# Kernel optimization log

Hardware: AMD Instinct MI355X
Metric: run time of the kernel (lower is better)

Reference implementation:

```python
import jax, jax.numpy as jnp
from jax import lax
import numpy as np

BS, HID, INP, NSPAN, NOUT, NUM_DAYS = 4096, 1024, 512, 8, 2, 20


def setup_inputs() -> dict:
    key = jax.random.key(0)
    ks = jax.random.split(key, 12)
    s = 1.0 / np.sqrt(HID)  # torch default uniform(-1/sqrt(hid), 1/sqrt(hid))
    u = lambda k, shape: jax.random.uniform(k, shape, jnp.float32, -s, s)
    return {
        "hx": jax.random.normal(ks[0], (BS, HID), jnp.float32),
        "cx": jax.random.normal(ks[1], (BS, HID), jnp.float32),
        "W_ih": u(ks[2], (4 * HID, INP)),
        "W_hh": u(ks[3], (4 * HID, HID)),
        "b_ih": u(ks[4], (4 * HID,)),
        "b_hh": u(ks[5], (4 * HID,)),
        "W_fcin": u(ks[6], (INP, HID)),
        "b_fcin": u(ks[7], (INP,)),
        "W_fcout": u(ks[8], (NOUT, HID)),
        "b_fcout": u(ks[9], (NOUT,)),
        "W_span": u(ks[10], (NSPAN, HID)),
        "b_span": u(ks[11], (NSPAN,)),
    }


def reference(hx, cx, W_ih, W_hh, b_ih, b_hh, W_fcin, b_fcin, W_fcout, b_fcout, W_span, b_span):
    # num-span head on the initial hidden state
    num_spans = jax.nn.softmax(hx @ W_span.T + b_span, axis=-1)  # [B, NSPAN]

    def step(carry, _):
        h, c, inp = carry
        gates = inp @ W_ih.T + b_ih + h @ W_hh.T + b_hh  # [B, 4H]
        i, f, g, o = jnp.split(gates, 4, axis=-1)  # torch LSTMCell gate order i,f,g,o
        c = jax.nn.sigmoid(f) * c + jax.nn.sigmoid(i) * jnp.tanh(g)
        h = jax.nn.sigmoid(o) * jnp.tanh(c)
        inp = jax.nn.relu(h @ W_fcin.T + b_fcin)  # next-step input
        out = jax.nn.softmax(h @ W_fcout.T + b_fcout, axis=-1)  # [B, 2]
        return (h, c, inp), out

    inp0 = jnp.zeros((hx.shape[0], W_ih.shape[1]), hx.dtype)
    _, outs = lax.scan(step, (hx, cx, inp0), None, length=NUM_DAYS)  # [T, B, 2]
    outputs = jnp.transpose(outs, (1, 0, 2))  # [B, T, 2]
    return num_spans, outputs
```

## Files before the change

kernel.cpp:

```cpp
#include <hip/hip_runtime.h>

typedef __bf16 bf16x8 __attribute__((ext_vector_type(8)));
typedef float f32x4 __attribute__((ext_vector_type(4)));
typedef unsigned short ushort_t;
typedef unsigned short u16x8 __attribute__((ext_vector_type(8)));

#define BSZ 4096
#define HID 1024
#define INPD 512
#define NSPAN 8
#define NOUT 2
#define NDAYS 20
#define XLD 1536


__device__ __forceinline__ ushort_t f2bf(float f) {
  union { float f; unsigned u; } v; v.f = f;
  unsigned r = v.u + 0x7FFFu + ((v.u >> 16) & 1u);
  return (ushort_t)(r >> 16);
}
__device__ __forceinline__ float bf2f(ushort_t b) {
  union { unsigned u; float f; } v; v.u = ((unsigned)b) << 16;
  return v.f;
}
__device__ __forceinline__ float sigf(float x) { return 1.f / (1.f + __expf(-x)); }
__device__ __forceinline__ float tanhfast(float x) { return 2.f / (1.f + __expf(-2.f * x)) - 1.f; }

__device__ __forceinline__ void gload16(const void* g, void* l) {
  __builtin_amdgcn_global_load_lds((const __attribute__((address_space(1))) void*)g,
                                   (__attribute__((address_space(3))) void*)l, 16, 0, 0);
}

__global__ void prep_gates_w(const float* __restrict__ Wih, const float* __restrict__ Whh,
                             const float* __restrict__ bih, const float* __restrict__ bhh,
                             ushort_t* __restrict__ Wgf, float* __restrict__ bg) {
  int gid = blockIdx.x * 256 + threadIdx.x;
  int rb = gid / 3072;
  int rem = gid - rb * 3072;
  int kk = rem >> 6;
  int li = rem & 63;
  int rp = rb * 16 + (li & 15);
  int kb = kk * 32 + ((li >> 4) << 3);
  int g = (rp >> 4) & 3;
  int j = (rp >> 6) * 16 + (rp & 15);
  int src = g * HID + j;
  const float* s = (kb < INPD) ? (Wih + (size_t)src * INPD + kb)
                               : (Whh + (size_t)src * HID + (kb - INPD));
  u16x8 o;
#pragma unroll
  for (int e = 0; e < 8; ++e) o[e] = f2bf(s[e]);
  *(u16x8*)(Wgf + (size_t)gid * 8) = o;
  if (kk == 0 && li < 16) bg[rp] = bih[src] + bhh[src];
}

__global__ void prep_fcin_w(const float* __restrict__ W, ushort_t* __restrict__ Wf) {
  int gid = blockIdx.x * 256 + threadIdx.x;
  int rb = gid / 2048;
  int rem = gid - rb * 2048;
  int kk = rem >> 6;
  int li = rem & 63;
  int row = rb * 16 + (li & 15);
  int kb = kk * 32 + ((li >> 4) << 3);
  const float* s = W + (size_t)row * HID + kb;
  u16x8 o;
#pragma unroll
  for (int e = 0; e < 8; ++e) o[e] = f2bf(s[e]);
  *(u16x8*)(Wf + (size_t)gid * 8) = o;
}

__global__ void init_x(const float* __restrict__ hx, ushort_t* __restrict__ Xf) {
  int gid = blockIdx.x * 256 + threadIdx.x;
  int rb = gid / 3072;
  int rem = gid - rb * 3072;
  int kk = rem >> 6;
  int li = rem & 63;
  int row = rb * 16 + (li & 15);
  int kb = kk * 32 + ((li >> 4) << 3);
  u16x8 o;
  if (kb < INPD) {
#pragma unroll
    for (int e = 0; e < 8; ++e) o[e] = 0;
  } else {
    const float* s = hx + (size_t)row * HID + (kb - INPD);
#pragma unroll
    for (int e = 0; e < 8; ++e) o[e] = f2bf(s[e]);
  }
  *(u16x8*)(Xf + (size_t)gid * 8) = o;
}

__global__ void span_kernel(const float* __restrict__ hx, const float* __restrict__ Wspan,
                            const float* __restrict__ bspan, float* __restrict__ out) {
  int gid = blockIdx.x * 256 + threadIdx.x;
  int b = gid >> 3, o = gid & 7;
  const float4* hr = (const float4*)(hx + (size_t)b * HID);
  const float4* wr = (const float4*)(Wspan + (size_t)o * HID);
  float acc = 0.f;
  for (int i = 0; i < HID / 4; ++i) {
    float4 h = hr[i], w = wr[i];
    acc += h.x * w.x + h.y * w.y + h.z * w.z + h.w * w.w;
  }
  acc += bspan[o];
  float m = acc;
  for (int s = 1; s < 8; s <<= 1) m = fmaxf(m, __shfl_xor(m, s));
  float e = __expf(acc - m);
  float ssum = e;
  for (int s = 1; s < 8; s <<= 1) ssum += __shfl_xor(ssum, s);
  out[gid] = e / ssum;
}

__global__ void fcout_kernel(const ushort_t* __restrict__ Xf, const float* __restrict__ W,
                             const float* __restrict__ bvec, float* __restrict__ outp, int t) {
  const int lane = threadIdx.x & 63;
  const int wave = threadIdx.x >> 6;
  const int b = blockIdx.x * 4 + wave;
  const int rb = b >> 4, r = b & 15;
  const int kk = 16 + (lane >> 1);
  const int ss = (lane & 1) * 2;
  const size_t base = ((size_t)rb * 48 + kk) * 512 + (ss * 16 + r) * 8;
  u16x8 h0 = *(const u16x8*)(Xf + base);
  u16x8 h1 = *(const u16x8*)(Xf + base + 128);
  const float* w0 = W + lane * 16;
  const float* w1 = W + HID + lane * 16;
  float l0 = 0.f, l1 = 0.f;
#pragma unroll
  for (int j = 0; j < 8; ++j) {
    float ha = bf2f(h0[j]);
    l0 += ha * w0[j];
    l1 += ha * w1[j];
    float hb = bf2f(h1[j]);
    l0 += hb * w0[j + 8];
    l1 += hb * w1[j + 8];
  }
#pragma unroll
  for (int s = 32; s > 0; s >>= 1) {
    l0 += __shfl_xor(l0, s);
    l1 += __shfl_xor(l1, s);
  }
  if (lane == 0) {
    l0 += bvec[0];
    l1 += bvec[1];
    float m = fmaxf(l0, l1);
    float e0 = __expf(l0 - m), e1 = __expf(l1 - m);
    float inv = 1.f / (e0 + e1);
    float* o = outp + (size_t)b * (NDAYS * NOUT) + t * NOUT;
    o[0] = e0 * inv;
    o[1] = e1 * inv;
  }
}

__global__ void gates128_kernel(const ushort_t* __restrict__ A,
                                const ushort_t* __restrict__ B,
                                const float* __restrict__ bias, float* __restrict__ cbuf,
                                ushort_t* __restrict__ hout) {
  __shared__ __align__(16) ushort_t ldsA[8 * 512];
  __shared__ __align__(16) ushort_t ldsB[8 * 512];
  const int tid = threadIdx.x;
  const int lane = tid & 63;
  const int wave = tid >> 6;

  int bid = blockIdx.y * gridDim.x + blockIdx.x;
  int nwg = gridDim.x * gridDim.y;
  int cpx = nwg >> 3;
  int swz = (bid & 7) * cpx + (bid >> 3);
  int bx = swz % gridDim.x;
  int by = swz / gridDim.x;
  const int bm = bx * 128;
  const int bn = by * 128;
  const int wm = (wave >> 1) * 64;
  const int wn = (wave & 1) * 64;

  f32x4 acc[4][4] = {};

  const int f0 = wave * 2, f1 = wave * 2 + 1;
  const ushort_t* gA0 = A + ((size_t)((bm >> 4) + f0) * 48) * 512 + lane * 8;
  const ushort_t* gA1 = A + ((size_t)((bm >> 4) + f1) * 48) * 512 + lane * 8;
  const ushort_t* gB0 = B + ((size_t)((bn >> 4) + f0) * 48) * 512 + lane * 8;
  const ushort_t* gB1 = B + ((size_t)((bn >> 4) + f1) * 48) * 512 + lane * 8;

  for (int kk = 0; kk < 48; ++kk) {
    const int ko = kk * 512;
    gload16(gA0 + ko, ldsA + f0 * 512);
    gload16(gA1 + ko, ldsA + f1 * 512);
    gload16(gB0 + ko, ldsB + f0 * 512);
    gload16(gB1 + ko, ldsB + f1 * 512);
    __syncthreads();

    bf16x8 af[4], bf[4];
#pragma unroll
    for (int i = 0; i < 4; ++i) {
      af[i] = *(const bf16x8*)(ldsA + ((wm >> 4) + i) * 512 + lane * 8);
      bf[i] = *(const bf16x8*)(ldsB + ((wn >> 4) + i) * 512 + lane * 8);
    }
#pragma unroll
    for (int mi = 0; mi < 4; ++mi)
#pragma unroll
      for (int ni = 0; ni < 4; ++ni)
        acc[mi][ni] = __builtin_amdgcn_mfma_f32_16x16x32_bf16(af[mi], bf[ni], acc[mi][ni], 0, 0, 0);
    __syncthreads();
  }

  const int colbase = bn + wn;
  const int jj = (colbase >> 6) * 16 + (lane & 15);
  const int cb = colbase + (lane & 15);
  const float bI = bias[cb];
  const float bF = bias[cb + 16];
  const float bG = bias[cb + 32];
  const float bO = bias[cb + 48];
  const size_t kpart = (size_t)(16 + (jj >> 5)) * 512 + ((jj & 31) >> 3) * 128 + (jj & 7);
  const int q4 = (lane >> 4) << 2;
#pragma unroll
  for (int mi = 0; mi < 4; ++mi) {
    const size_t rowbase = (size_t)(((bm + wm) >> 4) + mi) * 24576 + kpart;
#pragma unroll
    for (int r = 0; r < 4; ++r) {
      const int b = bm + wm + mi * 16 + q4 + r;
      float ig = sigf(acc[mi][0][r] + bI);
      float fg = sigf(acc[mi][1][r] + bF);
      float gg = tanhfast(acc[mi][2][r] + bG);
      float og = sigf(acc[mi][3][r] + bO);
      size_t cidx = (size_t)b * HID + jj;
      float cn = fg * cbuf[cidx] + ig * gg;
      cbuf[cidx] = cn;
      hout[rowbase + (q4 + r) * 8] = f2bf(og * tanhfast(cn));
    }
  }
}

__global__ void fcin64_kernel(const ushort_t* __restrict__ Xf,
                              const ushort_t* __restrict__ B,
                              const float* __restrict__ bias, ushort_t* __restrict__ hout,
                              const float* __restrict__ Wout, const float* __restrict__ bout,
                              float* __restrict__ outp, int t) {
  __shared__ __align__(16) ushort_t ldsA[2][4 * 512];
  __shared__ __align__(16) ushort_t ldsB[2][8 * 512];
  __shared__ float ldsW[2048];
  const int tid = threadIdx.x;
  const int lane = tid & 63;
  const int wave = tid >> 6;
  const int wmi = wave >> 1;
  const int wni = wave & 1;

  int bid = blockIdx.y * gridDim.x + blockIdx.x;
  int nwg = gridDim.x * gridDim.y;
  int cpx = nwg >> 3;
  int swz = (bid & 7) * cpx + (bid >> 3);
  int bx = swz % gridDim.x;
  int by = swz / gridDim.x;
  const int bm = bx * 64;
  const int bn = by * 128;
  const bool doOut = (by == 0);

  {
    float4 w0 = *(const float4*)(Wout + tid * 8);
    float4 w1 = *(const float4*)(Wout + tid * 8 + 4);
    *(float4*)(ldsW + tid * 8) = w0;
    *(float4*)(ldsW + tid * 8 + 4) = w1;
  }

  f32x4 acc[2][4] = {};
  float lo0 = 0.f, lo1 = 0.f;
  const int orow = tid >> 2, okq = tid & 3;
  const int ofr = orow >> 4, orw = orow & 15;

  const ushort_t* gA = Xf + ((size_t)((bm >> 4) + wave) * 48 + 16) * 512 + lane * 8;
  const ushort_t* gB0 = B + ((size_t)((bn >> 4) + 2 * wave) * 32) * 512 + lane * 8;
  const ushort_t* gB1 = B + ((size_t)((bn >> 4) + 2 * wave + 1) * 32) * 512 + lane * 8;

  gload16(gA, &ldsA[0][wave * 512]);
  gload16(gB0, &ldsB[0][(2 * wave) * 512]);
  gload16(gB1, &ldsB[0][(2 * wave + 1) * 512]);
  gload16(gA + 512, &ldsA[1][wave * 512]);
  gload16(gB0 + 512, &ldsB[1][(2 * wave) * 512]);
  gload16(gB1 + 512, &ldsB[1][(2 * wave + 1) * 512]);
  asm volatile("s_waitcnt vmcnt(3) lgkmcnt(0)" ::: "memory");
  __builtin_amdgcn_sched_barrier(0);
  __builtin_amdgcn_s_barrier();

  for (int kk = 0; kk < 32; ++kk) {
    const int cur = kk & 1;
    const ushort_t* lA = ldsA[cur];
    const ushort_t* lB = ldsB[cur];

    bf16x8 af[2], bf[4];
#pragma unroll
    for (int m = 0; m < 2; ++m)
      af[m] = *(const bf16x8*)(lA + (wmi * 2 + m) * 512 + lane * 8);
#pragma unroll
    for (int n = 0; n < 4; ++n)
      bf[n] = *(const bf16x8*)(lB + (wni * 4 + n) * 512 + lane * 8);

    if (doOut) {
      u16x8 h = *(const u16x8*)(lA + ofr * 512 + (okq * 16 + orw) * 8);
      const float* w0 = ldsW + kk * 32 + okq * 8;
      const float* w1 = ldsW + 1024 + kk * 32 + okq * 8;
#pragma unroll
      for (int e = 0; e < 8; ++e) {
        float hv = bf2f(h[e]);
        lo0 += hv * w0[e];
        lo1 += hv * w1[e];
      }
    }

    asm volatile("s_waitcnt lgkmcnt(0)" ::: "memory");
    __builtin_amdgcn_sched_barrier(0);
    __builtin_amdgcn_s_barrier();

    if (kk + 2 < 32) {
      const int ko = (kk + 2) * 512;
      gload16(gA + ko, &ldsA[cur][wave * 512]);
      gload16(gB0 + ko, &ldsB[cur][(2 * wave) * 512]);
      gload16(gB1 + ko, &ldsB[cur][(2 * wave + 1) * 512]);
    }

    __builtin_amdgcn_s_setprio(1);
#pragma unroll
    for (int m = 0; m < 2; ++m)
#pragma unroll
      for (int n = 0; n < 4; ++n)
        acc[m][n] = __builtin_amdgcn_mfma_f32_16x16x32_bf16(af[m], bf[n], acc[m][n], 0, 0, 0);
    __builtin_amdgcn_s_setprio(0);

    if (kk + 2 < 32) {
      asm volatile("s_waitcnt vmcnt(3)" ::: "memory");
    } else if (kk == 30) {
      asm volatile("s_waitcnt vmcnt(0)" ::: "memory");
    }
    __builtin_amdgcn_sched_barrier(0);
    if (kk < 31) __builtin_amdgcn_s_barrier();
  }

  const int q4 = (lane >> 4) << 2;
#pragma unroll
  for (int mi = 0; mi < 2; ++mi) {
    const size_t rowbase = (size_t)((bm >> 4) + wmi * 2 + mi) * 24576;
#pragma unroll
    for (int ni = 0; ni < 4; ++ni) {
      const int n = bn + wni * 64 + ni * 16 + (lane & 15);
      const float bb = bias[n];
      const size_t kpart = (size_t)(n >> 5) * 512 + ((n & 31) >> 3) * 128 + (n & 7);
#pragma unroll
      for (int r = 0; r < 4; ++r) {
        float v = fmaxf(acc[mi][ni][r] + bb, 0.f);
        hout[rowbase + kpart + (q4 + r) * 8] = f2bf(v);
      }
    }
  }

  if (doOut) {
    lo0 += __shfl_xor(lo0, 1);
    lo1 += __shfl_xor(lo1, 1);
    lo0 += __shfl_xor(lo0, 2);
    lo1 += __shfl_xor(lo1, 2);
    if (okq == 0) {
      float l0 = lo0 + bout[0];
      float l1 = lo1 + bout[1];
      float m = fmaxf(l0, l1);
      float e0 = __expf(l0 - m), e1 = __expf(l1 - m);
      float inv = 1.f / (e0 + e1);
      float* o = outp + (size_t)(bm + orow) * (NDAYS * NOUT) + t * NOUT;
      o[0] = e0 * inv;
      o[1] = e1 * inv;
    }
  }
}

extern "C" void kernel_launch(void* const* d_in, const int* in_sizes, int n_in, void* d_out,
                              int out_size, void* d_ws, size_t ws_size, hipStream_t stream) {
  const float* hx = (const float*)d_in[0];
  const float* cx = (const float*)d_in[1];
  const float* Wih = (const float*)d_in[2];
  const float* Whh = (const float*)d_in[3];
  const float* bih = (const float*)d_in[4];
  const float* bhh = (const float*)d_in[5];
  const float* Wfcin = (const float*)d_in[6];
  const float* bfcin = (const float*)d_in[7];
  const float* Wfcout = (const float*)d_in[8];
  const float* bfcout = (const float*)d_in[9];
  const float* Wspan = (const float*)d_in[10];
  const float* bspan = (const float*)d_in[11];
  float* out = (float*)d_out;

  char* ws = (char*)d_ws;
  ushort_t* Wgf = (ushort_t*)(ws);
  ushort_t* Wfcf = (ushort_t*)(ws + 12582912);
  float* bg = (float*)(ws + 13631488);
  ushort_t* XA = (ushort_t*)(ws + 13647872);
  ushort_t* XB = (ushort_t*)(ws + 26230784);
  float* cbuf = (float*)(ws + 38813696);

  prep_gates_w<<<3072, 256, 0, stream>>>(Wih, Whh, bih, bhh, Wgf, bg);
  prep_fcin_w<<<256, 256, 0, stream>>>(Wfcin, Wfcf);
  init_x<<<3072, 256, 0, stream>>>(hx, XA);
  hipMemcpyAsync(cbuf, cx, (size_t)BSZ * HID * 4, hipMemcpyDeviceToDevice, stream);
  span_kernel<<<(BSZ * NSPAN) / 256, 256, 0, stream>>>(hx, Wspan, bspan, out);

  float* outp = out + BSZ * NSPAN;
  for (int t = 0; t < NDAYS; ++t) {
    ushort_t* Xin = (t & 1) ? XB : XA;
    ushort_t* Xout = (t & 1) ? XA : XB;
    gates128_kernel<<<dim3(32, 32), 256, 0, stream>>>(Xin, Wgf, bg, cbuf, Xout);
    if (t < NDAYS - 1) {
      fcin64_kernel<<<dim3(64, 4), 256, 0, stream>>>(Xout, Wfcf, bfcin, Xout,
                                                     Wfcout, bfcout, outp, t);
    } else {
      fcout_kernel<<<BSZ / 4, 256, 0, stream>>>(Xout, Wfcout, bfcout, outp, t);
    }
  }
}
```

Baseline: 1.554 ms.

## Replace 128x128 gates GEMM with double-buffered 256x256 ping-pong pipelined kernel

Rewrites the fused LSTM gates GEMM to use 256x256 tiles with 8 waves and 512 threads. It double-buffers LDS and interleaves global-to-LDS staging with MFMA phases, using explicit barriers, vmcnt waits and setprio. The aim is more data reuse per tile and hiding load latency behind compute, instead of fully synchronising on every K chunk. In exchange the grid shrinks to 256 workgroups, about one per CU at occupancy 1. Register pressure is also high from the 8x4 accumulators.

Measured after the change: 1.540 ms. Within noise of the previous version (-0.9%).

```diff
diff --git a/kernel.cpp b/kernel.cpp
--- a/kernel.cpp
+++ b/kernel.cpp
@@ -148,58 +148,120 @@
   }
 }
 
-__global__ void gates128_kernel(const ushort_t* __restrict__ A,
-                                const ushort_t* __restrict__ B,
-                                const float* __restrict__ bias, float* __restrict__ cbuf,
-                                ushort_t* __restrict__ hout) {
-  __shared__ __align__(16) ushort_t ldsA[8 * 512];
-  __shared__ __align__(16) ushort_t ldsB[8 * 512];
+#define RD_A(BUFA, MH)                                                            \
+  _Pragma("unroll") for (int m_ = 0; m_ < 4; ++m_)                                \
+  _Pragma("unroll") for (int kk_ = 0; kk_ < 2; ++kk_)                             \
+    af[m_][kk_] = *(const bf16x8*)&BUFA[(((wmi8 + (MH)*4 + m_) * 2 + kk_) << 9) + lane8];
+
+#define RD_B(BUFB, NH)                                                            \
+  _Pragma("unroll") for (int n_ = 0; n_ < 2; ++n_)                                \
+  _Pragma("unroll") for (int kk_ = 0; kk_ < 2; ++kk_)                             \
+    bfr[(NH)*2 + n_][kk_] = *(const bf16x8*)&BUFB[(((wni4 + (NH)*2 + n_) * 2 + kk_) << 9) + lane8];
+
+#define DO_MFMA(MH, NH)                                                           \
+  __builtin_amdgcn_s_setprio(1);                                                  \
+  _Pragma("unroll") for (int m_ = 0; m_ < 4; ++m_)                                \
+  _Pragma("unroll") for (int n_ = 0; n_ < 2; ++n_)                                \
+  _Pragma("unroll") for (int kk_ = 0; kk_ < 2; ++kk_)                             \
+    acc[(MH)*4 + m_][(NH)*2 + n_] = __builtin_amdgcn_mfma_f32_16x16x32_bf16(      \
+        af[m_][kk_], bfr[(NH)*2 + n_][kk_], acc[(MH)*4 + m_][(NH)*2 + n_], 0, 0, 0); \
+  __builtin_amdgcn_s_setprio(0);
+
+__global__ __launch_bounds__(512, 1) void gates256_kernel(
+    const ushort_t* __restrict__ A, const ushort_t* __restrict__ B,
+    const float* __restrict__ bias, float* __restrict__ cbuf,
+    ushort_t* __restrict__ hout) {
+  __shared__ __align__(16) ushort_t ldsA[2][16384];
+  __shared__ __align__(16) ushort_t ldsB[2][16384];
   const int tid = threadIdx.x;
   const int lane = tid & 63;
   const int wave = tid >> 6;
-
-  int bid = blockIdx.y * gridDim.x + blockIdx.x;
-  int nwg = gridDim.x * gridDim.y;
-  int cpx = nwg >> 3;
-  int swz = (bid & 7) * cpx + (bid >> 3);
-  int bx = swz % gridDim.x;
-  int by = swz / gridDim.x;
-  const int bm = bx * 128;
-  const int bn = by * 128;
-  const int wm = (wave >> 1) * 64;
-  const int wn = (wave & 1) * 64;
-
-  f32x4 acc[4][4] = {};
-
-  const int f0 = wave * 2, f1 = wave * 2 + 1;
-  const ushort_t* gA0 = A + ((size_t)((bm >> 4) + f0) * 48) * 512 + lane * 8;
-  const ushort_t* gA1 = A + ((size_t)((bm >> 4) + f1) * 48) * 512 + lane * 8;
-  const ushort_t* gB0 = B + ((size_t)((bn >> 4) + f0) * 48) * 512 + lane * 8;
-  const ushort_t* gB1 = B + ((size_t)((bn >> 4) + f1) * 48) * 512 + lane * 8;
-
-  for (int kk = 0; kk < 48; ++kk) {
-    const int ko = kk * 512;
-    gload16(gA0 + ko, ldsA + f0 * 512);
-    gload16(gA1 + ko, ldsA + f1 * 512);
-    gload16(gB0 + ko, ldsB + f0 * 512);
-    gload16(gB1 + ko, ldsB + f1 * 512);
-    __syncthreads();
-
-    bf16x8 af[4], bf[4];
-#pragma unroll
-    for (int i = 0; i < 4; ++i) {
-      af[i] = *(const bf16x8*)(ldsA + ((wm >> 4) + i) * 512 + lane * 8);
-      bf[i] = *(const bf16x8*)(ldsB + ((wn >> 4) + i) * 512 + lane * 8);
-    }
-#pragma unroll
-    for (int mi = 0; mi < 4; ++mi)
-#pragma unroll
-      for (int ni = 0; ni < 4; ++ni)
-        acc[mi][ni] = __builtin_amdgcn_mfma_f32_16x16x32_bf16(af[mi], bf[ni], acc[mi][ni], 0, 0, 0);
-    __syncthreads();
-  }
-
-  const int colbase = bn + wn;
+  const int wmi = wave >> 2;
+  const int wni = wave & 3;
+  const int wmi8 = wmi * 8, wni4 = wni * 4, lane8 = lane * 8;
+
+  const int bid = blockIdx.y * 16 + blockIdx.x;
+  const int swz = (bid & 7) * 32 + (bid >> 3);
+  const int bm = (swz & 15) * 256;
+  const int bn = (swz >> 4) * 256;
+
+  const int fl0 = tid >> 6;
+  const int srb = fl0 >> 1;
+  const int skk = fl0 & 1;
+  const ushort_t* gA0 = A + (((size_t)((bm >> 4) + srb) * 48 + skk) << 9) + ((tid & 63) << 3);
+  const ushort_t* gB0 = B + (((size_t)((bn >> 4) + srb) * 48 + skk) << 9) + ((tid & 63) << 3);
+
+  auto STAGE_A = [&](int buf, int tt, int h) {
+    const size_t o = (((size_t)h * 384) + (size_t)tt * 2) << 9;
+    gload16(gA0 + o, &ldsA[buf][h * 8192 + tid * 8]);
+    gload16(gA0 + o + ((size_t)192 << 9), &ldsA[buf][h * 8192 + 4096 + tid * 8]);
+  };
+  auto STAGE_B = [&](int buf, int tt, int h) {
+    const size_t o = (((size_t)h * 384) + (size_t)tt * 2) << 9;
+    gload16(gB0 + o, &ldsB[buf][h * 8192 + tid * 8]);
+    gload16(gB0 + o + ((size_t)192 << 9), &ldsB[buf][h * 8192 + 4096 + tid * 8]);
+  };
+
+  f32x4 acc[8][4] = {};
+  bf16x8 af[4][2];
+  bf16x8 bfr[4][2];
+
+  STAGE_A(0, 0, 0); STAGE_A(0, 0, 1); STAGE_B(0, 0, 0); STAGE_B(0, 0, 1);
+  STAGE_A(1, 1, 0); STAGE_A(1, 1, 1); STAGE_B(1, 1, 0); STAGE_B(1, 1, 1);
+  asm volatile("s_waitcnt vmcnt(8)" ::: "memory");
+  __builtin_amdgcn_sched_barrier(0);
+  __builtin_amdgcn_s_barrier();
+
+  for (int i = 0; i < 12; ++i) {
+    const bool stg = (i <= 10);
+    RD_A(ldsA[0], 0); RD_B(ldsB[0], 0);
+    if (i >= 1) STAGE_A(1, 2 * i + 1, 0);
+    __builtin_amdgcn_s_barrier();
+    DO_MFMA(0, 0);
+    __builtin_amdgcn_s_barrier();
+    RD_B(ldsB[0], 1);
+    if (i >= 1) STAGE_A(1, 2 * i + 1, 1);
+    __builtin_amdgcn_s_barrier();
+    DO_MFMA(0, 1);
+    __builtin_amdgcn_s_barrier();
+    RD_A(ldsA[0], 1);
+    if (stg) STAGE_B(0, 2 * i + 2, 0);
+    __builtin_amdgcn_s_barrier();
+    DO_MFMA(1, 0);
+    __builtin_amdgcn_s_barrier();
+    if (stg) STAGE_B(0, 2 * i + 2, 1);
+    __builtin_amdgcn_s_barrier();
+    DO_MFMA(1, 1);
+    if (i < 11) asm volatile("s_waitcnt vmcnt(4)" ::: "memory");
+    else        asm volatile("s_waitcnt vmcnt(0)" ::: "memory");
+    __builtin_amdgcn_sched_barrier(0);
+    __builtin_amdgcn_s_barrier();
+    RD_A(ldsA[1], 0); RD_B(ldsB[1], 0);
+    if (stg) STAGE_A(0, 2 * i + 2, 0);
+    __builtin_amdgcn_s_barrier();
+    DO_MFMA(0, 0);
+    __builtin_amdgcn_s_barrier();
+    RD_B(ldsB[1], 1);
+    if (stg) STAGE_A(0, 2 * i + 2, 1);
+    __builtin_amdgcn_s_barrier();
+    DO_MFMA(0, 1);
+    __builtin_amdgcn_s_barrier();
+    RD_A(ldsA[1], 1);
+    if (stg) STAGE_B(1, 2 * i + 3, 0);
+    __builtin_amdgcn_s_barrier();
+    DO_MFMA(1, 0);
+    __builtin_amdgcn_s_barrier();
+    if (stg) STAGE_B(1, 2 * i + 3, 1);
+    __builtin_amdgcn_s_barrier();
+    DO_MFMA(1, 1);
+    if (i < 11) {
+      asm volatile("s_waitcnt vmcnt(4)" ::: "memory");
+      __builtin_amdgcn_sched_barrier(0);
+    }
+    __builtin_amdgcn_s_barrier();
+  }
+
+  const int colbase = bn + wni * 64;
   const int jj = (colbase >> 6) * 16 + (lane & 15);
   const int cb = colbase + (lane & 15);
   const float bI = bias[cb];
@@ -209,15 +271,15 @@
   const size_t kpart = (size_t)(16 + (jj >> 5)) * 512 + ((jj & 31) >> 3) * 128 + (jj & 7);
   const int q4 = (lane >> 4) << 2;
 #pragma unroll
-  for (int mi = 0; mi < 4; ++mi) {
-    const size_t rowbase = (size_t)(((bm + wm) >> 4) + mi) * 24576 + kpart;
+  for (int m = 0; m < 8; ++m) {
+    const size_t rowbase = (size_t)((bm >> 4) + wmi * 8 + m) * 24576 + kpart;
 #pragma unroll
     for (int r = 0; r < 4; ++r) {
-      const int b = bm + wm + mi * 16 + q4 + r;
-      float ig = sigf(acc[mi][0][r] + bI);
-      float fg = sigf(acc[mi][1][r] + bF);
-      float gg = tanhfast(acc[mi][2][r] + bG);
-      float og = sigf(acc[mi][3][r] + bO);
+      const int b = bm + wmi * 128 + m * 16 + q4 + r;
+      float ig = sigf(acc[m][0][r] + bI);
+      float fg = sigf(acc[m][1][r] + bF);
+      float gg = tanhfast(acc[m][2][r] + bG);
+      float og = sigf(acc[m][3][r] + bO);
       size_t cidx = (size_t)b * HID + jj;
       float cn = fg * cbuf[cidx] + ig * gg;
       cbuf[cidx] = cn;
@@ -398,7 +460,7 @@
   for (int t = 0; t < NDAYS; ++t) {
     ushort_t* Xin = (t & 1) ? XB : XA;
     ushort_t* Xout = (t & 1) ? XA : XB;
-    gates128_kernel<<<dim3(32, 32), 256, 0, stream>>>(Xin, Wgf, bg, cbuf, Xout);
+    gates256_kernel<<<dim3(16, 16), 512, 0, stream>>>(Xin, Wgf, bg, cbuf, Xout);
     if (t < NDAYS - 1) {
       fcin64_kernel<<<dim3(64, 4), 256, 0, stream>>>(Xout, Wfcf, bfcin, Xout,
                                                      Wfcout, bfcout, outp, t);
```
